# Performance work log

Measured on AMD Instinct MI355X. Metric: run time of the kernel, lower is better.

## Reference

```python
import jax, jax.numpy as jnp
import numpy as np

N_NODES = 10000
N_EDGES = 320000
NFEAT, NHID, NCLASS = 512, 256, 40


def setup_inputs() -> dict:
    key = jax.random.key(0)
    ks = jax.random.split(key, 8)
    x = jax.random.normal(ks[0], (N_NODES, NFEAT), dtype=jnp.float32)
    edge_src = jax.random.randint(ks[1], (N_EDGES,), 0, N_NODES, dtype=jnp.int32)
    edge_dst = jax.random.randint(ks[2], (N_EDGES,), 0, N_NODES, dtype=jnp.int32)
    edge_w = jax.random.uniform(ks[3], (N_EDGES,), dtype=jnp.float32)
    W1 = jax.random.normal(ks[4], (NFEAT, NHID), dtype=jnp.float32) * (1.0 / np.sqrt(NFEAT))
    b1 = jax.random.normal(ks[5], (NHID,), dtype=jnp.float32) * 0.01
    W2 = jax.random.normal(ks[6], (NHID, NCLASS), dtype=jnp.float32) * (1.0 / np.sqrt(NHID))
    b2 = jax.random.normal(ks[7], (NCLASS,), dtype=jnp.float32) * 0.01
    return {"x": x, "edge_src": edge_src, "edge_dst": edge_dst, "edge_w": edge_w,
            "W1": W1, "b1": b1, "W2": W2, "b2": b2}


def _spmm(edge_src, edge_dst, edge_w, h):
    # out[i] = sum_{e: dst_e == i} w_e * h[src_e]   (sparse adj @ h)
    msgs = h[edge_src] * edge_w[:, None]            # [E, d]
    return jax.ops.segment_sum(msgs, edge_dst, num_segments=h.shape[0])


def reference(x, edge_src, edge_dst, edge_w, W1, b1, W2, b2):
    # Layer 1: GraphConvolution(nfeat->nhid) with ReLU (dropout = identity in eval)
    h = jax.nn.relu(_spmm(edge_src, edge_dst, edge_w, x @ W1) + b1)
    # Layer 2: GraphConvolution(nhid->nclass), identity activation
    out = _spmm(edge_src, edge_dst, edge_w, h @ W2) + b2
    return jax.nn.log_softmax(out, axis=1)
```

## Files before the change

### kernel.cpp

```cpp
#include <hip/hip_runtime.h>
#include <hip/hip_bf16.h>
#include <math.h>

#define N_NODES 10000
#define MPAD    10112
#define N_EDGES 320000
#define NFEAT   512
#define NHID    256
#define NCLASS  40
#define SLOT    96
#define EB      ((N_EDGES + 255) / 256)
#define G1X     (MPAD / 128)
#define G1Y     (NHID / 64)

typedef short  short8  __attribute__((ext_vector_type(8)));
typedef float  floatx4 __attribute__((ext_vector_type(4)));

__device__ __forceinline__ unsigned short f2b(float f) {
  __hip_bfloat16 h = __float2bfloat16(f);
  unsigned short u; __builtin_memcpy(&u, &h, 2); return u;
}
__device__ __forceinline__ float b2f(unsigned short u) {
  return __uint_as_float(((unsigned)u) << 16);
}


__global__ __launch_bounds__(256) void prep_k(const float* __restrict__ x,
                                              const float* __restrict__ W1,
                                              const float* __restrict__ W2,
                                              unsigned short* __restrict__ xb,
                                              unsigned short* __restrict__ w1t,
                                              unsigned short* __restrict__ w2t,
                                              int* __restrict__ cnt) {
  int tid = blockIdx.x * 256 + threadIdx.x;
  if (tid < N_NODES) cnt[tid] = 0;
  const int nx4 = MPAD * NFEAT / 4;
  const int nw1 = NFEAT * NHID;
  if (tid < nx4) {
    int i = tid * 4;
    int row = i / NFEAT;
    float4 v = make_float4(0.f, 0.f, 0.f, 0.f);
    if (row < N_NODES) v = *(const float4*)&x[i];
    ushort4 o;
    o.x = f2b(v.x); o.y = f2b(v.y); o.z = f2b(v.z); o.w = f2b(v.w);
    *(ushort4*)&xb[i] = o;
  } else if (tid < nx4 + nw1) {
    int j = tid - nx4;
    int k = j / NHID, n = j % NHID;
    w1t[n * NFEAT + k] = f2b(W1[j]);
  } else {
    int j = tid - nx4 - nw1;
    if (j < 64 * NHID) {
      int n = j >> 8;
      int k = j & 255;
      w2t[j] = (n < NCLASS) ? f2b(W2[k * NCLASS + n]) : (unsigned short)0;
    }
  }
}


__global__ __launch_bounds__(256) void scatter_gemm1_k(
    const int* __restrict__ src, const int* __restrict__ dst,
    const float* __restrict__ w, int* __restrict__ cnt, int2* __restrict__ epk,
    const unsigned short* __restrict__ xb, const unsigned short* __restrict__ w1t,
    unsigned short* __restrict__ xw1b) {
  if (blockIdx.x < EB) {
    int e = blockIdx.x * 256 + threadIdx.x;
    if (e < N_EDGES) {
      int d = dst[e];
      int p = atomicAdd(&cnt[d], 1);
      int2 pk; pk.x = src[e]; pk.y = __float_as_int(w[e]);
      epk[d * SLOT + p] = pk;
    }
    return;
  }
  __shared__ short8 As[128 * 4];
  __shared__ short8 Bs[64 * 4];

  const int b  = blockIdx.x - EB;
  const int bx = b % G1X;
  const int by = b / G1X;
  const int bm = bx * 128;
  const int bn = by * 64;
  const int t  = threadIdx.x;
  const int l  = t & 63;
  const int wv = t >> 6;
  const int wr = wv >> 1, wc = wv & 1;

  const int rowA = t >> 1, sA = (t & 1) * 2;
  const int rowB = t >> 2, sB = t & 3;

  const floatx4 zero = {0.f, 0.f, 0.f, 0.f};
  floatx4 acc[4][2];
#pragma unroll
  for (int mi = 0; mi < 4; mi++) { acc[mi][0] = zero; acc[mi][1] = zero; }

  const int q = l >> 4;

  for (int k0 = 0; k0 < NFEAT; k0 += 32) {
    short8 a0 = *(const short8*)&xb [(size_t)(bm + rowA) * NFEAT + k0 + sA * 8];
    short8 a1 = *(const short8*)&xb [(size_t)(bm + rowA) * NFEAT + k0 + sA * 8 + 8];
    short8 bv = *(const short8*)&w1t[(size_t)(bn + rowB) * NFEAT + k0 + sB * 8];
    __syncthreads();
    As[rowA * 4 + ((sA    ) ^ (rowA & 3))] = a0;
    As[rowA * 4 + ((sA + 1) ^ (rowA & 3))] = a1;
    Bs[rowB * 4 + (sB ^ (rowB & 3))] = bv;
    __syncthreads();

    short8 af[4], bf2[2];
#pragma unroll
    for (int mi = 0; mi < 4; mi++) {
      int ar = wr * 64 + mi * 16 + (l & 15);
      af[mi] = As[ar * 4 + (q ^ (ar & 3))];
    }
#pragma unroll
    for (int ni = 0; ni < 2; ni++) {
      int bc = wc * 32 + ni * 16 + (l & 15);
      bf2[ni] = Bs[bc * 4 + (q ^ (bc & 3))];
    }
#pragma unroll
    for (int mi = 0; mi < 4; mi++)
#pragma unroll
      for (int ni = 0; ni < 2; ni++)
        acc[mi][ni] = __builtin_amdgcn_mfma_f32_16x16x32_bf16(af[mi], bf2[ni], acc[mi][ni], 0, 0, 0);
  }

#pragma unroll
  for (int mi = 0; mi < 4; mi++)
#pragma unroll
    for (int ni = 0; ni < 2; ni++) {
      int row = bm + wr * 64 + mi * 16 + (l >> 4) * 4;
      int col = bn + wc * 32 + ni * 16 + (l & 15);
#pragma unroll
      for (int r = 0; r < 4; r++)
        xw1b[(size_t)(row + r) * NHID + col] = f2b(acc[mi][ni][r]);
    }
}


__global__ __launch_bounds__(256) void spmm1_k(const int* __restrict__ cnt,
                                               const int2* __restrict__ epk,
                                               const unsigned short* __restrict__ xw1b,
                                               const float* __restrict__ b1,
                                               unsigned short* __restrict__ h) {
  int bid     = blockIdx.x;
  int xcd     = bid & 7;
  int slice   = xcd >> 2;
  int quarter = xcd & 3;
  int wave    = threadIdx.x >> 6;
  int lane    = threadIdx.x & 63;
  int node    = (bid >> 3) * 4 + wave + quarter * 2500;
  int f0      = slice * 128 + lane * 2;

  int e0 = node * SLOT;
  int n  = cnt[node];
  float accx = 0.f, accy = 0.f;
  for (int base = 0; base < n; base += 64) {
    int c2 = n - base; if (c2 > 64) c2 = 64;
    int2 my = make_int2(0, 0);
    if (lane < c2) my = epk[e0 + base + lane];
    int j = 0;
    for (; j + 8 <= c2; j += 8) {
      int   s0 = __shfl(my.x, j + 0); float w0 = __int_as_float(__shfl(my.y, j + 0));
      int   s1 = __shfl(my.x, j + 1); float w1 = __int_as_float(__shfl(my.y, j + 1));
      int   s2 = __shfl(my.x, j + 2); float w2 = __int_as_float(__shfl(my.y, j + 2));
      int   s3 = __shfl(my.x, j + 3); float w3 = __int_as_float(__shfl(my.y, j + 3));
      int   s4 = __shfl(my.x, j + 4); float w4 = __int_as_float(__shfl(my.y, j + 4));
      int   s5 = __shfl(my.x, j + 5); float w5 = __int_as_float(__shfl(my.y, j + 5));
      int   s6 = __shfl(my.x, j + 6); float w6 = __int_as_float(__shfl(my.y, j + 6));
      int   s7 = __shfl(my.x, j + 7); float w7 = __int_as_float(__shfl(my.y, j + 7));
      unsigned v0 = *(const unsigned*)&xw1b[(size_t)s0 * NHID + f0];
      unsigned v1 = *(const unsigned*)&xw1b[(size_t)s1 * NHID + f0];
      unsigned v2 = *(const unsigned*)&xw1b[(size_t)s2 * NHID + f0];
      unsigned v3 = *(const unsigned*)&xw1b[(size_t)s3 * NHID + f0];
      unsigned v4 = *(const unsigned*)&xw1b[(size_t)s4 * NHID + f0];
      unsigned v5 = *(const unsigned*)&xw1b[(size_t)s5 * NHID + f0];
      unsigned v6 = *(const unsigned*)&xw1b[(size_t)s6 * NHID + f0];
      unsigned v7 = *(const unsigned*)&xw1b[(size_t)s7 * NHID + f0];
      accx = fmaf(w0, b2f((unsigned short)(v0 & 0xffff)), accx);
      accy = fmaf(w0, b2f((unsigned short)(v0 >> 16)),    accy);
      accx = fmaf(w1, b2f((unsigned short)(v1 & 0xffff)), accx);
      accy = fmaf(w1, b2f((unsigned short)(v1 >> 16)),    accy);
      accx = fmaf(w2, b2f((unsigned short)(v2 & 0xffff)), accx);
      accy = fmaf(w2, b2f((unsigned short)(v2 >> 16)),    accy);
      accx = fmaf(w3, b2f((unsigned short)(v3 & 0xffff)), accx);
      accy = fmaf(w3, b2f((unsigned short)(v3 >> 16)),    accy);
      accx = fmaf(w4, b2f((unsigned short)(v4 & 0xffff)), accx);
      accy = fmaf(w4, b2f((unsigned short)(v4 >> 16)),    accy);
      accx = fmaf(w5, b2f((unsigned short)(v5 & 0xffff)), accx);
      accy = fmaf(w5, b2f((unsigned short)(v5 >> 16)),    accy);
      accx = fmaf(w6, b2f((unsigned short)(v6 & 0xffff)), accx);
      accy = fmaf(w6, b2f((unsigned short)(v6 >> 16)),    accy);
      accx = fmaf(w7, b2f((unsigned short)(v7 & 0xffff)), accx);
      accy = fmaf(w7, b2f((unsigned short)(v7 >> 16)),    accy);
    }
    for (; j < c2; j++) {
      int   sj = __shfl(my.x, j);
      float wj = __int_as_float(__shfl(my.y, j));
      unsigned v = *(const unsigned*)&xw1b[(size_t)sj * NHID + f0];
      accx = fmaf(wj, b2f((unsigned short)(v & 0xffff)), accx);
      accy = fmaf(wj, b2f((unsigned short)(v >> 16)),    accy);
    }
  }
  accx += b1[f0];
  accy += b1[f0 + 1];
  unsigned po = ((unsigned)f2b(fmaxf(accy, 0.f)) << 16) | f2b(fmaxf(accx, 0.f));
  *(unsigned*)&h[(size_t)node * NHID + f0] = po;
}


__global__ __launch_bounds__(256) void gemm2_k(const unsigned short* __restrict__ h,
                                               const unsigned short* __restrict__ w2t,
                                               float* __restrict__ hw2) {
  __shared__ short8 As[64 * 4];
  __shared__ short8 Bs[64 * 4];

  const int t  = threadIdx.x;
  const int bm = blockIdx.x * 64;
  const int l  = t & 63;
  const int wv = t >> 6;
  const int wr = wv >> 1, wc = wv & 1;
  const int srow = t >> 2, sslot = t & 3;

  const floatx4 zero = {0.f, 0.f, 0.f, 0.f};
  floatx4 acc[2][2];
  acc[0][0] = zero; acc[0][1] = zero; acc[1][0] = zero; acc[1][1] = zero;

  const int q = l >> 4;

  for (int k0 = 0; k0 < NHID; k0 += 32) {
    short8 av = *(const short8*)&h  [(size_t)(bm + srow) * NHID + k0 + sslot * 8];
    short8 bv = *(const short8*)&w2t[(size_t)srow * NHID + k0 + sslot * 8];
    __syncthreads();
    As[srow * 4 + (sslot ^ (srow & 3))] = av;
    Bs[srow * 4 + (sslot ^ (srow & 3))] = bv;
    __syncthreads();

    short8 af[2], bf2[2];
#pragma unroll
    for (int mi = 0; mi < 2; mi++) {
      int ar = wr * 32 + mi * 16 + (l & 15);
      af[mi] = As[ar * 4 + (q ^ (ar & 3))];
    }
#pragma unroll
    for (int ni = 0; ni < 2; ni++) {
      int bc = wc * 32 + ni * 16 + (l & 15);
      bf2[ni] = Bs[bc * 4 + (q ^ (bc & 3))];
    }
#pragma unroll
    for (int mi = 0; mi < 2; mi++)
#pragma unroll
      for (int ni = 0; ni < 2; ni++)
        acc[mi][ni] = __builtin_amdgcn_mfma_f32_16x16x32_bf16(af[mi], bf2[ni], acc[mi][ni], 0, 0, 0);
  }

#pragma unroll
  for (int mi = 0; mi < 2; mi++)
#pragma unroll
    for (int ni = 0; ni < 2; ni++) {
      int row = bm + wr * 32 + mi * 16 + (l >> 4) * 4;
      int col = wc * 32 + ni * 16 + (l & 15);
#pragma unroll
      for (int r = 0; r < 4; r++)
        hw2[(size_t)(row + r) * 64 + col] = acc[mi][ni][r];
    }
}


__global__ __launch_bounds__(256) void spmm2_k(const int* __restrict__ cnt,
                                               const int2* __restrict__ epk,
                                               const float* __restrict__ hw2,
                                               const float* __restrict__ b2,
                                               float* __restrict__ out) {
  int wave = threadIdx.x >> 6;
  int lane = threadIdx.x & 63;
  int i    = blockIdx.x * 4 + wave;
  bool act = (lane < NCLASS);
  int e0 = i * SLOT;
  int n  = cnt[i];
  float acc = act ? b2[lane] : 0.f;
  for (int base = 0; base < n; base += 64) {
    int c2 = n - base; if (c2 > 64) c2 = 64;
    int2 my = make_int2(0, 0);
    if (lane < c2) my = epk[e0 + base + lane];
    int j = 0;
    for (; j + 8 <= c2; j += 8) {
      int   s0 = __shfl(my.x, j + 0); float w0 = __int_as_float(__shfl(my.y, j + 0));
      int   s1 = __shfl(my.x, j + 1); float w1 = __int_as_float(__shfl(my.y, j + 1));
      int   s2 = __shfl(my.x, j + 2); float w2 = __int_as_float(__shfl(my.y, j + 2));
      int   s3 = __shfl(my.x, j + 3); float w3 = __int_as_float(__shfl(my.y, j + 3));
      int   s4 = __shfl(my.x, j + 4); float w4 = __int_as_float(__shfl(my.y, j + 4));
      int   s5 = __shfl(my.x, j + 5); float w5 = __int_as_float(__shfl(my.y, j + 5));
      int   s6 = __shfl(my.x, j + 6); float w6 = __int_as_float(__shfl(my.y, j + 6));
      int   s7 = __shfl(my.x, j + 7); float w7 = __int_as_float(__shfl(my.y, j + 7));
      if (act) {
        float v0 = hw2[(size_t)s0 * 64 + lane];
        float v1 = hw2[(size_t)s1 * 64 + lane];
        float v2 = hw2[(size_t)s2 * 64 + lane];
        float v3 = hw2[(size_t)s3 * 64 + lane];
        float v4 = hw2[(size_t)s4 * 64 + lane];
        float v5 = hw2[(size_t)s5 * 64 + lane];
        float v6 = hw2[(size_t)s6 * 64 + lane];
        float v7 = hw2[(size_t)s7 * 64 + lane];
        acc = fmaf(w0, v0, acc); acc = fmaf(w1, v1, acc);
        acc = fmaf(w2, v2, acc); acc = fmaf(w3, v3, acc);
        acc = fmaf(w4, v4, acc); acc = fmaf(w5, v5, acc);
        acc = fmaf(w6, v6, acc); acc = fmaf(w7, v7, acc);
      }
    }
    for (; j < c2; j++) {
      int   sj = __shfl(my.x, j);
      float wj = __int_as_float(__shfl(my.y, j));
      if (act) acc = fmaf(wj, hw2[(size_t)sj * 64 + lane], acc);
    }
  }
  float v = act ? acc : -INFINITY;
#pragma unroll
  for (int o = 32; o > 0; o >>= 1) v = fmaxf(v, __shfl_xor(v, o));
  float m  = v;
  float ex = act ? expf(acc - m) : 0.f;
  float s  = ex;
#pragma unroll
  for (int o = 32; o > 0; o >>= 1) s += __shfl_xor(s, o);
  float ls = logf(s);
  if (act) out[(size_t)i * NCLASS + lane] = acc - m - ls;
}


static inline size_t align256(size_t v) { return (v + 255) & ~(size_t)255; }

extern "C" void kernel_launch(void* const* d_in, const int* in_sizes, int n_in,
                              void* d_out, int out_size, void* d_ws, size_t ws_size,
                              hipStream_t stream) {
  const float* x        = (const float*)d_in[0];
  const int*   edge_src = (const int*)  d_in[1];
  const int*   edge_dst = (const int*)  d_in[2];
  const float* edge_w   = (const float*)d_in[3];
  const float* W1       = (const float*)d_in[4];
  const float* b1       = (const float*)d_in[5];
  const float* W2       = (const float*)d_in[6];
  const float* b2       = (const float*)d_in[7];
  float* out = (float*)d_out;

  char* ws = (char*)d_ws;
  size_t off = 0;
  unsigned short* xb   = (unsigned short*)(ws + off); off = align256(off + (size_t)MPAD * NFEAT * 2);
  unsigned short* w1t  = (unsigned short*)(ws + off); off = align256(off + (size_t)NFEAT * NHID * 2);
  unsigned short* w2t  = (unsigned short*)(ws + off); off = align256(off + (size_t)64 * NHID * 2);
  unsigned short* xw1b = (unsigned short*)(ws + off); off = align256(off + (size_t)MPAD * NHID * 2);
  unsigned short* h    = (unsigned short*)(ws + off); off = align256(off + (size_t)MPAD * NHID * 2);
  float* hw2 = (float*)(ws + off); off = align256(off + (size_t)MPAD * 64 * 4);
  int*   cnt = (int*)  (ws + off); off = align256(off + (size_t)N_NODES * 4);
  int2*  epk = (int2*) (ws + off); off = align256(off + (size_t)N_NODES * SLOT * 8);

  const int PREP_ITEMS = MPAD * NFEAT / 4 + NFEAT * NHID + 64 * NHID;
  prep_k<<<(PREP_ITEMS + 255) / 256, 256, 0, stream>>>(x, W1, W2, xb, w1t, w2t, cnt);

  scatter_gemm1_k<<<EB + G1X * G1Y, 256, 0, stream>>>(edge_src, edge_dst, edge_w,
                                                      cnt, epk, xb, w1t, xw1b);

  spmm1_k<<<5000, 256, 0, stream>>>(cnt, epk, xw1b, b1, h);

  gemm2_k<<<MPAD / 64, 256, 0, stream>>>(h, w2t, hw2);

  spmm2_k<<<2500, 256, 0, stream>>>(cnt, epk, hw2, b2, out);
}
```

Measured before the change: 82.06 us.

## Fuse x bf16 conversion into GEMM1, enlarge N tile, widen SpMM gathers

Drops the separate fp32-to-bf16 pass over x. GEMM1 now reads x in fp32 and packs it to bf16 in registers, which avoids writing and re-reading a bf16 copy. GEMM1 tiles grow from 128x64 to 128x128 and its blocks are placed before the edge-scatter blocks. Both SpMM kernels split each wave into two half-waves that take alternate edges with wider vector loads, then combine with a cross-half shuffle. The gemm2 grid changes from MPAD/64 (158) to 157 blocks, which risks leaving the last 64-row tile uncomputed unless gemm2's indexing also changed in code not shown.

```diff
diff --git a/kernel.cpp b/kernel.cpp
--- a/kernel.cpp
+++ b/kernel.cpp
@@ -11,7 +11,7 @@
 #define SLOT    96
 #define EB      ((N_EDGES + 255) / 256)
 #define G1X     (MPAD / 128)
-#define G1Y     (NHID / 64)
+#define NG1     (G1X * (NHID / 128))
 
 typedef short  short8  __attribute__((ext_vector_type(8)));
 typedef float  floatx4 __attribute__((ext_vector_type(4)));
@@ -23,33 +23,27 @@
 __device__ __forceinline__ float b2f(unsigned short u) {
   return __uint_as_float(((unsigned)u) << 16);
 }
-
-
-__global__ __launch_bounds__(256) void prep_k(const float* __restrict__ x,
-                                              const float* __restrict__ W1,
+__device__ __forceinline__ short8 pack8(float4 a, float4 b) {
+  short8 r;
+  r[0] = (short)f2b(a.x); r[1] = (short)f2b(a.y); r[2] = (short)f2b(a.z); r[3] = (short)f2b(a.w);
+  r[4] = (short)f2b(b.x); r[5] = (short)f2b(b.y); r[6] = (short)f2b(b.z); r[7] = (short)f2b(b.w);
+  return r;
+}
+
+
+__global__ __launch_bounds__(256) void prep_k(const float* __restrict__ W1,
                                               const float* __restrict__ W2,
-                                              unsigned short* __restrict__ xb,
                                               unsigned short* __restrict__ w1t,
                                               unsigned short* __restrict__ w2t,
                                               int* __restrict__ cnt) {
   int tid = blockIdx.x * 256 + threadIdx.x;
   if (tid < N_NODES) cnt[tid] = 0;
-  const int nx4 = MPAD * NFEAT / 4;
   const int nw1 = NFEAT * NHID;
-  if (tid < nx4) {
-    int i = tid * 4;
-    int row = i / NFEAT;
-    float4 v = make_float4(0.f, 0.f, 0.f, 0.f);
-    if (row < N_NODES) v = *(const float4*)&x[i];
-    ushort4 o;
-    o.x = f2b(v.x); o.y = f2b(v.y); o.z = f2b(v.z); o.w = f2b(v.w);
-    *(ushort4*)&xb[i] = o;
-  } else if (tid < nx4 + nw1) {
-    int j = tid - nx4;
-    int k = j / NHID, n = j % NHID;
-    w1t[n * NFEAT + k] = f2b(W1[j]);
+  if (tid < nw1) {
+    int k = tid / NHID, n = tid % NHID;
+    w1t[n * NFEAT + k] = f2b(W1[tid]);
   } else {
-    int j = tid - nx4 - nw1;
+    int j = tid - nw1;
     if (j < 64 * NHID) {
       int n = j >> 8;
       int k = j & 255;
@@ -59,13 +53,13 @@
 }
 
 
-__global__ __launch_bounds__(256) void scatter_gemm1_k(
+__global__ __launch_bounds__(256) void gemm1_scatter_k(
+    const float* __restrict__ x, const unsigned short* __restrict__ w1t,
+    unsigned short* __restrict__ xw1b,
     const int* __restrict__ src, const int* __restrict__ dst,
-    const float* __restrict__ w, int* __restrict__ cnt, int2* __restrict__ epk,
-    const unsigned short* __restrict__ xb, const unsigned short* __restrict__ w1t,
-    unsigned short* __restrict__ xw1b) {
-  if (blockIdx.x < EB) {
-    int e = blockIdx.x * 256 + threadIdx.x;
+    const float* __restrict__ w, int* __restrict__ cnt, int2* __restrict__ epk) {
+  if (blockIdx.x >= NG1) {
+    int e = (blockIdx.x - NG1) * 256 + threadIdx.x;
     if (e < N_EDGES) {
       int d = dst[e];
       int p = atomicAdd(&cnt[d], 1);
@@ -75,62 +69,74 @@
     return;
   }
   __shared__ short8 As[128 * 4];
-  __shared__ short8 Bs[64 * 4];
-
-  const int b  = blockIdx.x - EB;
+  __shared__ short8 Bs[128 * 4];
+
+  const int b  = blockIdx.x;
   const int bx = b % G1X;
   const int by = b / G1X;
   const int bm = bx * 128;
-  const int bn = by * 64;
+  const int bn = by * 128;
   const int t  = threadIdx.x;
   const int l  = t & 63;
   const int wv = t >> 6;
   const int wr = wv >> 1, wc = wv & 1;
 
-  const int rowA = t >> 1, sA = (t & 1) * 2;
-  const int rowB = t >> 2, sB = t & 3;
+  const int rowX = t >> 1;
+  const int sX   = (t & 1) * 2;
 
   const floatx4 zero = {0.f, 0.f, 0.f, 0.f};
-  floatx4 acc[4][2];
-#pragma unroll
-  for (int mi = 0; mi < 4; mi++) { acc[mi][0] = zero; acc[mi][1] = zero; }
+  floatx4 acc[4][4];
+#pragma unroll
+  for (int mi = 0; mi < 4; mi++)
+#pragma unroll
+    for (int ni = 0; ni < 4; ni++) acc[mi][ni] = zero;
 
   const int q = l >> 4;
 
   for (int k0 = 0; k0 < NFEAT; k0 += 32) {
-    short8 a0 = *(const short8*)&xb [(size_t)(bm + rowA) * NFEAT + k0 + sA * 8];
-    short8 a1 = *(const short8*)&xb [(size_t)(bm + rowA) * NFEAT + k0 + sA * 8 + 8];
-    short8 bv = *(const short8*)&w1t[(size_t)(bn + rowB) * NFEAT + k0 + sB * 8];
+    int arow = bm + rowX;
+    float4 xa0 = make_float4(0.f, 0.f, 0.f, 0.f), xa1 = xa0, xa2 = xa0, xa3 = xa0;
+    if (arow < N_NODES) {
+      const float* xp = &x[(size_t)arow * NFEAT + k0 + sX * 8];
+      xa0 = *(const float4*)(xp);
+      xa1 = *(const float4*)(xp + 4);
+      xa2 = *(const float4*)(xp + 8);
+      xa3 = *(const float4*)(xp + 12);
+    }
+    short8 a0 = pack8(xa0, xa1), a1 = pack8(xa2, xa3);
+    short8 b0 = *(const short8*)&w1t[(size_t)(bn + rowX) * NFEAT + k0 + sX * 8];
+    short8 b1v = *(const short8*)&w1t[(size_t)(bn + rowX) * NFEAT + k0 + sX * 8 + 8];
     __syncthreads();
-    As[rowA * 4 + ((sA    ) ^ (rowA & 3))] = a0;
-    As[rowA * 4 + ((sA + 1) ^ (rowA & 3))] = a1;
-    Bs[rowB * 4 + (sB ^ (rowB & 3))] = bv;
+    As[rowX * 4 + ((sX    ) ^ (rowX & 3))] = a0;
+    As[rowX * 4 + ((sX + 1) ^ (rowX & 3))] = a1;
+    Bs[rowX * 4 + ((sX    ) ^ (rowX & 3))] = b0;
+    Bs[rowX * 4 + ((sX + 1) ^ (rowX & 3))] = b1v;
     __syncthreads();
 
-    short8 af[4], bf2[2];
+    short8 af[4], bf[4];
 #pragma unroll
     for (int mi = 0; mi < 4; mi++) {
       int ar = wr * 64 + mi * 16 + (l & 15);
       af[mi] = As[ar * 4 + (q ^ (ar & 3))];
     }
 #pragma unroll
-    for (int ni = 0; ni < 2; ni++) {
-      int bc = wc * 32 + ni * 16 + (l & 15);
-      bf2[ni] = Bs[bc * 4 + (q ^ (bc & 3))];
+    for (int ni = 0; ni < 4; ni++) {
+      int bc = wc * 64 + ni * 16 + (l & 15);
+      bf[ni] = Bs[bc * 4 + (q ^ (bc & 3))];
     }
 #pragma unroll
     for (int mi = 0; mi < 4; mi++)
 #pragma unroll
-      for (int ni = 0; ni < 2; ni++)
-        acc[mi][ni] = __builtin_amdgcn_mfma_f32_16x16x32_bf16(af[mi], bf2[ni], acc[mi][ni], 0, 0, 0);
+      for (int ni = 0; ni < 4; ni++)
+        acc[mi][ni] = __builtin_amdgcn_mfma_f32_16x16x32_bf16(af[mi], bf[ni], acc[mi][ni], 0, 0, 0);
   }
 
 #pragma unroll
   for (int mi = 0; mi < 4; mi++)
 #pragma unroll
-    for (int ni = 0; ni < 2; ni++) {
+    for (int ni = 0; ni < 4; ni++) {
       int row = bm + wr * 64 + mi * 16 + (l >> 4) * 4;
-      int col = bn + wc * 32 + ni * 16 + (l & 15);
+      int col = bn + wc * 64 + ni * 16 + (l & 15);
 #pragma unroll
       for (int r = 0; r < 4; r++)
         xw1b[(size_t)(row + r) * NHID + col] = f2b(acc[mi][ni][r]);
@@ -150,62 +156,57 @@
   int wave    = threadIdx.x >> 6;
   int lane    = threadIdx.x & 63;
   int node    = (bid >> 3) * 4 + wave + quarter * 2500;
-  int f0      = slice * 128 + lane * 2;
+  int hh      = lane >> 5;
+  int f       = lane & 31;
+  int fbase   = slice * 128 + f * 4;
 
   int e0 = node * SLOT;
   int n  = cnt[node];
-  float accx = 0.f, accy = 0.f;
+  float a0 = 0.f, a1 = 0.f, a2 = 0.f, a3 = 0.f;
   for (int base = 0; base < n; base += 64) {
     int c2 = n - base; if (c2 > 64) c2 = 64;
     int2 my = make_int2(0, 0);
     if (lane < c2) my = epk[e0 + base + lane];
     int j = 0;
     for (; j + 8 <= c2; j += 8) {
-      int   s0 = __shfl(my.x, j + 0); float w0 = __int_as_float(__shfl(my.y, j + 0));
-      int   s1 = __shfl(my.x, j + 1); float w1 = __int_as_float(__shfl(my.y, j + 1));
-      int   s2 = __shfl(my.x, j + 2); float w2 = __int_as_float(__shfl(my.y, j + 2));
-      int   s3 = __shfl(my.x, j + 3); float w3 = __int_as_float(__shfl(my.y, j + 3));
-      int   s4 = __shfl(my.x, j + 4); float w4 = __int_as_float(__shfl(my.y, j + 4));
-      int   s5 = __shfl(my.x, j + 5); float w5 = __int_as_float(__shfl(my.y, j + 5));
-      int   s6 = __shfl(my.x, j + 6); float w6 = __int_as_float(__shfl(my.y, j + 6));
-      int   s7 = __shfl(my.x, j + 7); float w7 = __int_as_float(__shfl(my.y, j + 7));
-      unsigned v0 = *(const unsigned*)&xw1b[(size_t)s0 * NHID + f0];
-      unsigned v1 = *(const unsigned*)&xw1b[(size_t)s1 * NHID + f0];
-      unsigned v2 = *(const unsigned*)&xw1b[(size_t)s2 * NHID + f0];
-      unsigned v3 = *(const unsigned*)&xw1b[(size_t)s3 * NHID + f0];
-      unsigned v4 = *(const unsigned*)&xw1b[(size_t)s4 * NHID + f0];
-      unsigned v5 = *(const unsigned*)&xw1b[(size_t)s5 * NHID + f0];
-      unsigned v6 = *(const unsigned*)&xw1b[(size_t)s6 * NHID + f0];
-      unsigned v7 = *(const unsigned*)&xw1b[(size_t)s7 * NHID + f0];
-      accx = fmaf(w0, b2f((unsigned short)(v0 & 0xffff)), accx);
-      accy = fmaf(w0, b2f((unsigned short)(v0 >> 16)),    accy);
-      accx = fmaf(w1, b2f((unsigned short)(v1 & 0xffff)), accx);
-      accy = fmaf(w1, b2f((unsigned short)(v1 >> 16)),    accy);
-      accx = fmaf(w2, b2f((unsigned short)(v2 & 0xffff)), accx);
-      accy = fmaf(w2, b2f((unsigned short)(v2 >> 16)),    accy);
-      accx = fmaf(w3, b2f((unsigned short)(v3 & 0xffff)), accx);
-      accy = fmaf(w3, b2f((unsigned short)(v3 >> 16)),    accy);
-      accx = fmaf(w4, b2f((unsigned short)(v4 & 0xffff)), accx);
-      accy = fmaf(w4, b2f((unsigned short)(v4 >> 16)),    accy);
-      accx = fmaf(w5, b2f((unsigned short)(v5 & 0xffff)), accx);
-      accy = fmaf(w5, b2f((unsigned short)(v5 >> 16)),    accy);
-      accx = fmaf(w6, b2f((unsigned short)(v6 & 0xffff)), accx);
-      accy = fmaf(w6, b2f((unsigned short)(v6 >> 16)),    accy);
-      accx = fmaf(w7, b2f((unsigned short)(v7 & 0xffff)), accx);
-      accy = fmaf(w7, b2f((unsigned short)(v7 >> 16)),    accy);
+#pragma unroll
+      for (int p = 0; p < 4; p++) {
+        int   idx = j + 2 * p + hh;
+        int   s   = __shfl(my.x, idx);
+        float wj  = __int_as_float(__shfl(my.y, idx));
+        uint2 v = *(const uint2*)&xw1b[(size_t)s * NHID + fbase];
+        a0 = fmaf(wj, b2f((unsigned short)(v.x & 0xffff)), a0);
+        a1 = fmaf(wj, b2f((unsigned short)(v.x >> 16)),    a1);
+        a2 = fmaf(wj, b2f((unsigned short)(v.y & 0xffff)), a2);
+        a3 = fmaf(wj, b2f((unsigned short)(v.y >> 16)),    a3);
+      }
     }
     for (; j < c2; j++) {
-      int   sj = __shfl(my.x, j);
+      int   s  = __shfl(my.x, j);
       float wj = __int_as_float(__shfl(my.y, j));
-      unsigned v = *(const unsigned*)&xw1b[(size_t)sj * NHID + f0];
-      accx = fmaf(wj, b2f((unsigned short)(v & 0xffff)), accx);
-      accy = fmaf(wj, b2f((unsigned short)(v >> 16)),    accy);
-    }
-  }
-  accx += b1[f0];
-  accy += b1[f0 + 1];
-  unsigned po = ((unsigned)f2b(fmaxf(accy, 0.f)) << 16) | f2b(fmaxf(accx, 0.f));
-  *(unsigned*)&h[(size_t)node * NHID + f0] = po;
+      if (hh == 0) {
+        uint2 v = *(const uint2*)&xw1b[(size_t)s * NHID + fbase];
+        a0 = fmaf(wj, b2f((unsigned short)(v.x & 0xffff)), a0);
+        a1 = fmaf(wj, b2f((unsigned short)(v.x >> 16)),    a1);
+        a2 = fmaf(wj, b2f((unsigned short)(v.y & 0xffff)), a2);
+        a3 = fmaf(wj, b2f((unsigned short)(v.y >> 16)),    a3);
+      }
+    }
+  }
+  a0 += __shfl_xor(a0, 32);
+  a1 += __shfl_xor(a1, 32);
+  a2 += __shfl_xor(a2, 32);
+  a3 += __shfl_xor(a3, 32);
+  if (hh == 0) {
+    a0 = fmaxf(a0 + b1[fbase + 0], 0.f);
+    a1 = fmaxf(a1 + b1[fbase + 1], 0.f);
+    a2 = fmaxf(a2 + b1[fbase + 2], 0.f);
+    a3 = fmaxf(a3 + b1[fbase + 3], 0.f);
+    uint2 po;
+    po.x = ((unsigned)f2b(a1) << 16) | f2b(a0);
+    po.y = ((unsigned)f2b(a3) << 16) | f2b(a2);
+    *(uint2*)&h[(size_t)node * NHID + fbase] = po;
+  }
 }
 
 
@@ -275,55 +276,52 @@
   int wave = threadIdx.x >> 6;
   int lane = threadIdx.x & 63;
   int i    = blockIdx.x * 4 + wave;
-  bool act = (lane < NCLASS);
+  int hh   = lane >> 5;
+  int c    = lane & 31;
+  bool act = (c * 2 < NCLASS);
   int e0 = i * SLOT;
   int n  = cnt[i];
-  float acc = act ? b2[lane] : 0.f;
+  float a0 = 0.f, a1 = 0.f;
   for (int base = 0; base < n; base += 64) {
     int c2 = n - base; if (c2 > 64) c2 = 64;
     int2 my = make_int2(0, 0);
     if (lane < c2) my = epk[e0 + base + lane];
     int j = 0;
     for (; j + 8 <= c2; j += 8) {
-      int   s0 = __shfl(my.x, j + 0); float w0 = __int_as_float(__shfl(my.y, j + 0));
-      int   s1 = __shfl(my.x, j + 1); float w1 = __int_as_float(__shfl(my.y, j + 1));
-      int   s2 = __shfl(my.x, j + 2); float w2 = __int_as_float(__shfl(my.y, j + 2));
-      int   s3 = __shfl(my.x, j + 3); float w3 = __int_as_float(__shfl(my.y, j + 3));
-      int   s4 = __shfl(my.x, j + 4); float w4 = __int_as_float(__shfl(my.y, j + 4));
-      int   s5 = __shfl(my.x, j + 5); float w5 = __int_as_float(__shfl(my.y, j + 5));
-      int   s6 = __shfl(my.x, j + 6); float w6 = __int_as_float(__shfl(my.y, j + 6));
-      int   s7 = __shfl(my.x, j + 7); float w7 = __int_as_float(__shfl(my.y, j + 7));
-      if (act) {
-        float v0 = hw2[(size_t)s0 * 64 + lane];
-        float v1 = hw2[(size_t)s1 * 64 + lane];
-        float v2 = hw2[(size_t)s2 * 64 + lane];
-        float v3 = hw2[(size_t)s3 * 64 + lane];
-        float v4 = hw2[(size_t)s4 * 64 + lane];
-        float v5 = hw2[(size_t)s5 * 64 + lane];
-        float v6 = hw2[(size_t)s6 * 64 + lane];
-        float v7 = hw2[(size_t)s7 * 64 + lane];
-        acc = fmaf(w0, v0, acc); acc = fmaf(w1, v1, acc);
-        acc = fmaf(w2, v2, acc); acc = fmaf(w3, v3, acc);
-        acc = fmaf(w4, v4, acc); acc = fmaf(w5, v5, acc);
-        acc = fmaf(w6, v6, acc); acc = fmaf(w7, v7, acc);
+#pragma unroll
+      for (int p = 0; p < 4; p++) {
+        int   idx = j + 2 * p + hh;
+        int   s   = __shfl(my.x, idx);
+        float wj  = __int_as_float(__shfl(my.y, idx));
+        float2 v = *(const float2*)&hw2[(size_t)s * 64 + c * 2];
+        a0 = fmaf(wj, v.x, a0);
+        a1 = fmaf(wj, v.y, a1);
       }
     }
     for (; j < c2; j++) {
-      int   sj = __shfl(my.x, j);
+      int   s  = __shfl(my.x, j);
       float wj = __int_as_float(__shfl(my.y, j));
-      if (act) acc = fmaf(wj, hw2[(size_t)sj * 64 + lane], acc);
-    }
-  }
-  float v = act ? acc : -INFINITY;
-#pragma unroll
-  for (int o = 32; o > 0; o >>= 1) v = fmaxf(v, __shfl_xor(v, o));
-  float m  = v;
-  float ex = act ? expf(acc - m) : 0.f;
-  float s  = ex;
-#pragma unroll
-  for (int o = 32; o > 0; o >>= 1) s += __shfl_xor(s, o);
-  float ls = logf(s);
-  if (act) out[(size_t)i * NCLASS + lane] = acc - m - ls;
+      if (hh == 0) {
+        float2 v = *(const float2*)&hw2[(size_t)s * 64 + c * 2];
+        a0 = fmaf(wj, v.x, a0);
+        a1 = fmaf(wj, v.y, a1);
+      }
+    }
+  }
+  a0 += __shfl_xor(a0, 32);
+  a1 += __shfl_xor(a1, 32);
+  if (act) { a0 += b2[c * 2]; a1 += b2[c * 2 + 1]; }
+  float mv = act ? fmaxf(a0, a1) : -INFINITY;
+#pragma unroll
+  for (int o = 16; o > 0; o >>= 1) mv = fmaxf(mv, __shfl_xor(mv, o));
+  float ex = act ? (expf(a0 - mv) + expf(a1 - mv)) : 0.f;
+#pragma unroll
+  for (int o = 16; o > 0; o >>= 1) ex += __shfl_xor(ex, o);
+  float ls = logf(ex);
+  if (act && hh == 0) {
+    float2 o2; o2.x = a0 - mv - ls; o2.y = a1 - mv - ls;
+    *(float2*)&out[(size_t)i * NCLASS + c * 2] = o2;
+  }
 }
 
 
@@ -344,7 +342,6 @@
 
   char* ws = (char*)d_ws;
   size_t off = 0;
-  unsigned short* xb   = (unsigned short*)(ws + off); off = align256(off + (size_t)MPAD * NFEAT * 2);
   unsigned short* w1t  = (unsigned short*)(ws + off); off = align256(off + (size_t)NFEAT * NHID * 2);
   unsigned short* w2t  = (unsigned short*)(ws + off); off = align256(off + (size_t)64 * NHID * 2);
   unsigned short* xw1b = (unsigned short*)(ws + off); off = align256(off + (size_t)MPAD * NHID * 2);
@@ -353,15 +350,15 @@
   int*   cnt = (int*)  (ws + off); off = align256(off + (size_t)N_NODES * 4);
   int2*  epk = (int2*) (ws + off); off = align256(off + (size_t)N_NODES * SLOT * 8);
 
-  const int PREP_ITEMS = MPAD * NFEAT / 4 + NFEAT * NHID + 64 * NHID;
-  prep_k<<<(PREP_ITEMS + 255) / 256, 256, 0, stream>>>(x, W1, W2, xb, w1t, w2t, cnt);
-
-  scatter_gemm1_k<<<EB + G1X * G1Y, 256, 0, stream>>>(edge_src, edge_dst, edge_w,
-                                                      cnt, epk, xb, w1t, xw1b);
+  const int PREP_ITEMS = NFEAT * NHID + 64 * NHID;
+  prep_k<<<(PREP_ITEMS + 255) / 256, 256, 0, stream>>>(W1, W2, w1t, w2t, cnt);
+
+  gemm1_scatter_k<<<NG1 + EB, 256, 0, stream>>>(x, w1t, xw1b,
+                                                edge_src, edge_dst, edge_w, cnt, epk);
 
   spmm1_k<<<5000, 256, 0, stream>>>(cnt, epk, xw1b, b1, h);
 
-  gemm2_k<<<MPAD / 64, 256, 0, stream>>>(h, w2t, hw2);
+  gemm2_k<<<157, 256, 0, stream>>>(h, w2t, hw2);
 
   spmm2_k<<<2500, 256, 0, stream>>>(cnt, epk, hw2, b2, out);
 }
```

Result: faster. 78.55 us (-4.3%).
